# Kernel tuning notes

Hardware: AMD Instinct MI355X
Metric: run time of the kernel (lower is better)

Reference implementation:

```python
import jax, jax.numpy as jnp
import numpy as np


def setup_inputs() -> dict:
    key = jax.random.key(0)
    ks = jax.random.split(key, 9)
    B, S, I, H, O = 64, 2048, 256, 256, 256
    s_g = 1.0 / np.sqrt(I + H)  # torch Linear default init scale
    s_f = 1.0 / np.sqrt(H)
    return {
        "x": jax.random.normal(ks[0], (B, S, I), dtype=jnp.float32),
        "W_r": jax.random.normal(ks[1], (H, I + H), dtype=jnp.float32) * s_g,
        "b_r": jax.random.normal(ks[2], (H,), dtype=jnp.float32) * s_g,
        "W_z": jax.random.normal(ks[3], (H, I + H), dtype=jnp.float32) * s_g,
        "b_z": jax.random.normal(ks[4], (H,), dtype=jnp.float32) * s_g,
        "W_h": jax.random.normal(ks[5], (H, I + H), dtype=jnp.float32) * s_g,
        "b_h": jax.random.normal(ks[6], (H,), dtype=jnp.float32) * s_g,
        "W_fc": jax.random.normal(ks[7], (O, H), dtype=jnp.float32) * s_f,
        "b_fc": jax.random.normal(ks[8], (O,), dtype=jnp.float32) * s_f,
    }


def reference(x, W_r, b_r, W_z, b_z, W_h, b_h, W_fc, b_fc):
    B, S, I = x.shape
    H = W_r.shape[0]
    h0 = jnp.zeros((B, H), dtype=x.dtype)

    def step(h, x_t):
        comb = jnp.concatenate([x_t, h], axis=1)            # [B, I+H]
        r = jax.nn.sigmoid(comb @ W_r.T + b_r)              # reset gate
        z = jax.nn.sigmoid(comb @ W_z.T + b_z)              # update gate
        comb_r = jnp.concatenate([x_t, r * h], axis=1)
        h_tilde = jnp.tanh(comb_r @ W_h.T + b_h)
        h_new = (1.0 - z) * h + z * h_tilde
        return h_new, h_new

    # scan over time (strict sequential dependency), x as [S, B, I]
    h_last, hs = jax.lax.scan(step, h0, jnp.swapaxes(x, 0, 1))
    outputs = jnp.einsum('sbh,oh->bso', hs, W_fc) + b_fc    # [B, S, O]
    return outputs, h_last
```

## Files before the change

### kernel.cpp

```cpp
#include <hip/hip_runtime.h>
#include <hip/hip_bf16.h>
#include <hip/hip_fp16.h>

typedef unsigned short u16;
typedef unsigned int u32;
typedef __attribute__((ext_vector_type(8))) short bf16x8;
typedef __attribute__((ext_vector_type(4))) float f32x4;
typedef _Float16 __attribute__((ext_vector_type(2))) f16x2;

#define MFMA16(a, b, c) __builtin_amdgcn_mfma_f32_16x16x32_bf16((a), (b), (c), 0, 0, 0)

__device__ __forceinline__ float bflo(u32 u) { return __uint_as_float(u << 16); }
__device__ __forceinline__ float bfhi(u32 u) { return __uint_as_float(u & 0xffff0000u); }
__device__ __forceinline__ float bf1(u16 u) { return __uint_as_float(((u32)u) << 16); }
__device__ __forceinline__ u16 f2bf(float f) {
    __hip_bfloat16 b = __float2bfloat16(f);
    return __builtin_bit_cast(u16, b);
}

__device__ __forceinline__ int sniff_fp32(const void* Wr) {
    const uint4* p = (const uint4*)Wr;
    uint4 v = p[threadIdx.x & 15];
    u32 a[4] = {v.x, v.y, v.z, v.w};
    float m = 0.f;
#pragma unroll
    for (int i = 0; i < 4; ++i) {
        float lo = fabsf(bflo(a[i])), hi = fabsf(bfhi(a[i]));
        if (!(lo < 1e30f)) lo = 1e30f;
        if (!(hi < 1e30f)) hi = 1e30f;
        m = fmaxf(m, fmaxf(lo, hi));
    }
#pragma unroll
    for (int off = 32; off; off >>= 1) m = fmaxf(m, __shfl_xor(m, off, 64));
    return m > 100.f ? 1 : 0;
}

__device__ __forceinline__ bf16x8 load8bf(const void* base, size_t idx, int f32) {
    if (f32) {
        const float4* p = (const float4*)((const float*)base + idx);
        float4 v0 = p[0], v1 = p[1];
        bf16x8 r;
        r[0] = (short)f2bf(v0.x); r[1] = (short)f2bf(v0.y);
        r[2] = (short)f2bf(v0.z); r[3] = (short)f2bf(v0.w);
        r[4] = (short)f2bf(v1.x); r[5] = (short)f2bf(v1.y);
        r[6] = (short)f2bf(v1.z); r[7] = (short)f2bf(v1.w);
        return r;
    }
    return *(const bf16x8*)((const u16*)base + idx);
}

__device__ __forceinline__ void load8h(const void* base, size_t idx, int f32, f16x2* dst) {
    if (f32) {
        const float4* p = (const float4*)((const float*)base + idx);
        float4 v0 = p[0], v1 = p[1];
        dst[0] = f16x2{(_Float16)v0.x, (_Float16)v0.y};
        dst[1] = f16x2{(_Float16)v0.z, (_Float16)v0.w};
        dst[2] = f16x2{(_Float16)v1.x, (_Float16)v1.y};
        dst[3] = f16x2{(_Float16)v1.z, (_Float16)v1.w};
    } else {
        uint4 v = *(const uint4*)((const u16*)base + idx);
        dst[0] = f16x2{(_Float16)bflo(v.x), (_Float16)bfhi(v.x)};
        dst[1] = f16x2{(_Float16)bflo(v.y), (_Float16)bfhi(v.y)};
        dst[2] = f16x2{(_Float16)bflo(v.z), (_Float16)bfhi(v.z)};
        dst[3] = f16x2{(_Float16)bflo(v.w), (_Float16)bfhi(v.w)};
    }
}

__device__ __forceinline__ float load1f(const void* base, size_t idx, int f32) {
    return f32 ? ((const float*)base)[idx] : bf1(((const u16*)base)[idx]);
}

__global__ __launch_bounds__(256, 2) void gru_pre(
    const void* __restrict__ x,
    const void* __restrict__ Wr, const void* __restrict__ Wz, const void* __restrict__ Wh,
    const void* __restrict__ br, const void* __restrict__ bz, const void* __restrict__ bh,
    __half* __restrict__ gxc, int s0, int lgSc)
{
    const int f32 = sniff_fp32(Wr);
    const int tid = threadIdx.x;
    const int R0 = blockIdx.x * 64;

    __shared__ __align__(16) u16 As[64][264];

    {
        const int i = tid >> 2;
        const int kq = (tid & 3) * 64;
        const int m = R0 + i;
        const int b = m >> lgSc;
        const int sl = m & ((1 << lgSc) - 1);
        const size_t xbase = ((size_t)(b * 2048 + s0 + sl)) * 256 + kq;
        u16* dst = &As[i][kq];
        if (f32) {
            const float4* p = (const float4*)((const float*)x + xbase);
#pragma unroll
            for (int j = 0; j < 8; ++j) {
                float4 v0 = p[2 * j], v1 = p[2 * j + 1];
                uint4 o;
                o.x = ((u32)f2bf(v0.y) << 16) | f2bf(v0.x);
                o.y = ((u32)f2bf(v0.w) << 16) | f2bf(v0.z);
                o.z = ((u32)f2bf(v1.y) << 16) | f2bf(v1.x);
                o.w = ((u32)f2bf(v1.w) << 16) | f2bf(v1.z);
                *(uint4*)(dst + j * 8) = o;
            }
        } else {
            const uint4* p = (const uint4*)((const u16*)x + xbase);
#pragma unroll
            for (int j = 0; j < 8; ++j) *(uint4*)(dst + j * 8) = p[j];
        }
    }
    __syncthreads();

    const int wv = tid >> 6;
    const int lane = tid & 63;
    const int q = lane >> 4, l16 = lane & 15;

    for (int j = 0; j < 3; ++j) {
        const int gi = wv * 3 + j;
        const int g = gi >> 2;
        const int col0 = (gi & 3) * 64;
        const void* W    = (g == 0) ? Wr : ((g == 1) ? Wz : Wh);
        const void* bias = (g == 0) ? br : ((g == 1) ? bz : bh);
        const size_t wbase = (size_t)(col0 + l16) * 512 + q * 8;

        f32x4 acc[4][4];
#pragma unroll
        for (int mt = 0; mt < 4; ++mt)
#pragma unroll
            for (int nt = 0; nt < 4; ++nt) acc[mt][nt] = (f32x4){0, 0, 0, 0};

#pragma unroll
        for (int k0 = 0; k0 < 256; k0 += 32) {
            bf16x8 bfr[4];
#pragma unroll
            for (int nt = 0; nt < 4; ++nt)
                bfr[nt] = load8bf(W, wbase + (size_t)nt * 16 * 512 + k0, f32);
#pragma unroll
            for (int mt = 0; mt < 4; ++mt) {
                bf16x8 af = *(const bf16x8*)&As[mt * 16 + l16][k0 + q * 8];
#pragma unroll
                for (int nt = 0; nt < 4; ++nt)
                    acc[mt][nt] = MFMA16(af, bfr[nt], acc[mt][nt]);
            }
        }
#pragma unroll
        for (int nt = 0; nt < 4; ++nt) {
            const int col = col0 + nt * 16 + l16;
            const float bv = load1f(bias, col, f32);
#pragma unroll
            for (int mt = 0; mt < 4; ++mt)
#pragma unroll
                for (int r = 0; r < 4; ++r) {
                    const int row = R0 + mt * 16 + q * 4 + r;
                    gxc[(size_t)row * 768 + g * 256 + col] =
                        __float2half(acc[mt][nt][r] + bv);
                }
        }
    }
}

__device__ __forceinline__ float dot256(const f16x2* w, const _Float16* hp) {
    const uint4* hp4 = (const uint4*)hp;
    float a0 = 0.f, a1 = 0.f, a2 = 0.f, a3 = 0.f;
#pragma unroll
    for (int c = 0; c < 32; ++c) {
        uint4 hv = hp4[c];
        f16x2 h0 = __builtin_bit_cast(f16x2, hv.x);
        f16x2 h1 = __builtin_bit_cast(f16x2, hv.y);
        f16x2 h2 = __builtin_bit_cast(f16x2, hv.z);
        f16x2 h3 = __builtin_bit_cast(f16x2, hv.w);
#if __has_builtin(__builtin_amdgcn_fdot2)
        a0 = __builtin_amdgcn_fdot2(w[c * 4 + 0], h0, a0, false);
        a1 = __builtin_amdgcn_fdot2(w[c * 4 + 1], h1, a1, false);
        a2 = __builtin_amdgcn_fdot2(w[c * 4 + 2], h2, a2, false);
        a3 = __builtin_amdgcn_fdot2(w[c * 4 + 3], h3, a3, false);
#else
        a0 += (float)w[c*4+0][0] * (float)h0[0] + (float)w[c*4+0][1] * (float)h0[1];
        a1 += (float)w[c*4+1][0] * (float)h1[0] + (float)w[c*4+1][1] * (float)h1[1];
        a2 += (float)w[c*4+2][0] * (float)h2[0] + (float)w[c*4+2][1] * (float)h2[1];
        a3 += (float)w[c*4+3][0] * (float)h3[0] + (float)w[c*4+3][1] * (float)h3[1];
#endif
    }
    return (a0 + a1) + (a2 + a3);
}

__global__ __launch_bounds__(768, 3) void gru_scan(
    const __half* __restrict__ gxc,
    const void* __restrict__ Wr, const void* __restrict__ Wz, const void* __restrict__ Wh,
    float* __restrict__ h_state,
    void* __restrict__ outbase,
    int s0, int Sc, int first, int last)
{
    const int f32 = sniff_fp32(Wr);
    const int b = blockIdx.x;
    const int tid = threadIdx.x;
    const int g = tid >> 8;
    const int n = tid & 255;

    __shared__ __align__(16) _Float16 h_h[256];
    __shared__ __align__(16) _Float16 rh_h[256];
    __shared__ float h_f[256];
    __shared__ float z_f[256];

    const void* W = (g == 0) ? Wr : ((g == 1) ? Wz : Wh);
    f16x2 w[128];
#pragma unroll
    for (int c = 0; c < 32; ++c)
        load8h(W, (size_t)n * 512 + 256 + c * 8, f32, &w[c * 4]);

    if (g == 0) {
        float h0 = first ? 0.0f : h_state[b * 256 + n];
        h_f[n] = h0;
        h_h[n] = (_Float16)h0;
    }
    __syncthreads();

    const __half* gxp = gxc + (size_t)b * Sc * 768 + g * 256 + n;
    __half cur = gxp[0];

    for (int s = 0; s < Sc; ++s) {
        __half nxt = (s + 1 < Sc) ? gxp[(size_t)(s + 1) * 768] : cur;

        if (g < 2) {
            float acc = dot256(w, h_h);
            float pre = acc + __half2float(cur);
            pre = fminf(fmaxf(pre, -30.0f), 30.0f);
            float val = __fdividef(1.0f, 1.0f + __expf(-pre));
            if (g == 0) rh_h[n] = (_Float16)(val * h_f[n]);
            else        z_f[n] = val;
        }
        __syncthreads();

        if (g == 2) {
            float acc = dot256(w, rh_h);
            float pre = acc + __half2float(cur);
            pre = fminf(fmaxf(pre, -15.0f), 15.0f);
            float e = __expf(2.0f * pre);
            float ht = __fdividef(e - 1.0f, e + 1.0f);
            float hold = h_f[n];
            float zz = z_f[n];
            float hn = hold + zz * (ht - hold);
            h_f[n] = hn;
            h_h[n] = (_Float16)hn;
            const size_t oidx = (size_t)(b * 2048 + s0 + s) * 256 + n;
            if (f32) ((float*)outbase)[oidx] = hn;
            else     ((u16*)outbase)[oidx] = f2bf(hn);
            if (s == Sc - 1) {
                h_state[b * 256 + n] = hn;
                if (last) {
                    const size_t lidx = (size_t)33554432 + b * 256 + n;
                    if (f32) ((float*)outbase)[lidx] = hn;
                    else     ((u16*)outbase)[lidx] = f2bf(hn);
                }
            }
        }
        __syncthreads();
        cur = nxt;
    }
}

__global__ __launch_bounds__(256) void gru_proj(
    const void* __restrict__ Wfc, const void* __restrict__ bfc,
    const void* __restrict__ Wr_for_sniff,
    void* __restrict__ io)
{
    const int f32 = sniff_fp32(Wr_for_sniff);
    const int lane = threadIdx.x & 63;
    const int wave = threadIdx.x >> 6;
    const int q = lane >> 4, l16 = lane & 15;
    const int m0 = blockIdx.x * 64 + wave * 16;
    const size_t aidx = (size_t)(m0 + l16) * 256 + q * 8;
    const size_t widx = (size_t)l16 * 256 + q * 8;
    f32x4 acc[16];
#pragma unroll
    for (int t = 0; t < 16; ++t) acc[t] = (f32x4){0, 0, 0, 0};
#pragma unroll 2
    for (int k0 = 0; k0 < 256; k0 += 32) {
        bf16x8 af = load8bf(io, aidx + k0, f32);
#pragma unroll
        for (int t = 0; t < 16; ++t) {
            bf16x8 bfg = load8bf(Wfc, widx + (size_t)t * 16 * 256 + k0, f32);
            acc[t] = MFMA16(af, bfg, acc[t]);
        }
    }
#pragma unroll
    for (int t = 0; t < 16; ++t) {
        const int col = t * 16 + l16;
        const float bv = load1f(bfc, col, f32);
#pragma unroll
        for (int r = 0; r < 4; ++r) {
            const size_t oidx = (size_t)(m0 + q * 4 + r) * 256 + col;
            float v = acc[t][r] + bv;
            if (f32) ((float*)io)[oidx] = v;
            else     ((u16*)io)[oidx] = f2bf(v);
        }
    }
}

extern "C" void kernel_launch(void* const* d_in, const int* in_sizes, int n_in,
                              void* d_out, int out_size, void* d_ws, size_t ws_size,
                              hipStream_t stream) {
    (void)in_sizes; (void)n_in; (void)out_size;
    const void* x   = d_in[0];
    const void* Wr  = d_in[1];
    const void* br  = d_in[2];
    const void* Wz  = d_in[3];
    const void* bz  = d_in[4];
    const void* Wh  = d_in[5];
    const void* bh  = d_in[6];
    const void* Wfc = d_in[7];
    const void* bfc = d_in[8];

    float* h_state = (float*)d_ws;
    __half* gxc = (__half*)((char*)d_ws + 65536);

    int lgSc = 11;
    while (lgSc > 0 &&
           (size_t)65536 + (((size_t)64 << lgSc) * 768 * 2) > ws_size) --lgSc;
    const int Sc = 1 << lgSc;

    for (int s0 = 0; s0 < 2048; s0 += Sc) {
        gru_pre<<<Sc, 256, 0, stream>>>(x, Wr, Wz, Wh, br, bz, bh, gxc, s0, lgSc);
        gru_scan<<<64, 768, 0, stream>>>(gxc, Wr, Wz, Wh, h_state, d_out,
                                         s0, Sc, (s0 == 0) ? 1 : 0,
                                         (s0 + Sc == 2048) ? 1 : 0);
    }
    gru_proj<<<2048, 256, 0, stream>>>(Wfc, bfc, Wr, d_out);
}
```

Before: 4.120 ms.

## Batch 16 sequences per scan block with fp16 MFMA recurrent matvec

The recurrent scan now handles 16 batch rows per workgroup over 4 blocks, replacing the per-row fdot2 dot products with fp16 MFMA over register-resident weights. The input-gate precompute is laid out time-major so each block can double-buffer the next step's gate inputs into LDS. Hidden states are staged as fp16 in a workspace and projected per chunk. A one-time kernel converts all weights to fp16. Using only 4 workgroups cuts GPU parallelism to a handful of CUs, and switching the precompute from bf16 to fp16 changes numerical behaviour.

New measurement: 14.67 ms. 256% more time.

```diff
diff --git a/kernel.cpp b/kernel.cpp
--- a/kernel.cpp
+++ b/kernel.cpp
@@ -4,11 +4,10 @@
 
 typedef unsigned short u16;
 typedef unsigned int u32;
-typedef __attribute__((ext_vector_type(8))) short bf16x8;
 typedef __attribute__((ext_vector_type(4))) float f32x4;
-typedef _Float16 __attribute__((ext_vector_type(2))) f16x2;
-
-#define MFMA16(a, b, c) __builtin_amdgcn_mfma_f32_16x16x32_bf16((a), (b), (c), 0, 0, 0)
+typedef __attribute__((ext_vector_type(8))) _Float16 f16x8;
+
+#define MFMAH(a, b, c) __builtin_amdgcn_mfma_f32_16x16x32_f16((a), (b), (c), 0, 0, 0)
 
 __device__ __forceinline__ float bflo(u32 u) { return __uint_as_float(u << 16); }
 __device__ __forceinline__ float bfhi(u32 u) { return __uint_as_float(u & 0xffff0000u); }
@@ -17,6 +16,10 @@
     __hip_bfloat16 b = __float2bfloat16(f);
     return __builtin_bit_cast(u16, b);
 }
+__device__ __forceinline__ u16 f2h(float f) { return __builtin_bit_cast(u16, (_Float16)f); }
+__device__ __forceinline__ u32 pk2h(float a, float b) {
+    return (u32)f2h(a) | ((u32)f2h(b) << 16);
+}
 
 __device__ __forceinline__ int sniff_fp32(const void* Wr) {
     const uint4* p = (const uint4*)Wr;
@@ -35,77 +38,80 @@
     return m > 100.f ? 1 : 0;
 }
 
-__device__ __forceinline__ bf16x8 load8bf(const void* base, size_t idx, int f32) {
-    if (f32) {
-        const float4* p = (const float4*)((const float*)base + idx);
-        float4 v0 = p[0], v1 = p[1];
-        bf16x8 r;
-        r[0] = (short)f2bf(v0.x); r[1] = (short)f2bf(v0.y);
-        r[2] = (short)f2bf(v0.z); r[3] = (short)f2bf(v0.w);
-        r[4] = (short)f2bf(v1.x); r[5] = (short)f2bf(v1.y);
-        r[6] = (short)f2bf(v1.z); r[7] = (short)f2bf(v1.w);
-        return r;
-    }
-    return *(const bf16x8*)((const u16*)base + idx);
-}
-
-__device__ __forceinline__ void load8h(const void* base, size_t idx, int f32, f16x2* dst) {
-    if (f32) {
-        const float4* p = (const float4*)((const float*)base + idx);
-        float4 v0 = p[0], v1 = p[1];
-        dst[0] = f16x2{(_Float16)v0.x, (_Float16)v0.y};
-        dst[1] = f16x2{(_Float16)v0.z, (_Float16)v0.w};
-        dst[2] = f16x2{(_Float16)v1.x, (_Float16)v1.y};
-        dst[3] = f16x2{(_Float16)v1.z, (_Float16)v1.w};
-    } else {
-        uint4 v = *(const uint4*)((const u16*)base + idx);
-        dst[0] = f16x2{(_Float16)bflo(v.x), (_Float16)bfhi(v.x)};
-        dst[1] = f16x2{(_Float16)bflo(v.y), (_Float16)bfhi(v.y)};
-        dst[2] = f16x2{(_Float16)bflo(v.z), (_Float16)bfhi(v.z)};
-        dst[3] = f16x2{(_Float16)bflo(v.w), (_Float16)bfhi(v.w)};
-    }
-}
-
 __device__ __forceinline__ float load1f(const void* base, size_t idx, int f32) {
     return f32 ? ((const float*)base)[idx] : bf1(((const u16*)base)[idx]);
 }
 
-__global__ __launch_bounds__(256, 2) void gru_pre(
-    const void* __restrict__ x,
-    const void* __restrict__ Wr, const void* __restrict__ Wz, const void* __restrict__ Wh,
-    const void* __restrict__ br, const void* __restrict__ bz, const void* __restrict__ bh,
-    __half* __restrict__ gxc, int s0, int lgSc)
+__global__ void wconv(const void* __restrict__ Wr, const void* __restrict__ Wz,
+                      const void* __restrict__ Wh, const void* __restrict__ Wfc,
+                      u16* __restrict__ wf16)
 {
     const int f32 = sniff_fp32(Wr);
+    const int gid = blockIdx.x * 256 + threadIdx.x;
+    const int e = gid * 4;
+    const void* src;
+    int off;
+    if (e < 131072)      { src = Wr;  off = e; }
+    else if (e < 262144) { src = Wz;  off = e - 131072; }
+    else if (e < 393216) { src = Wh;  off = e - 262144; }
+    else                 { src = Wfc; off = e - 393216; }
+    uint2 o;
+    if (f32) {
+        float4 v = *(const float4*)((const float*)src + off);
+        o.x = pk2h(v.x, v.y);
+        o.y = pk2h(v.z, v.w);
+    } else {
+        uint2 v = *(const uint2*)((const u16*)src + off);
+        o.x = pk2h(bflo(v.x), bfhi(v.x));
+        o.y = pk2h(bflo(v.y), bfhi(v.y));
+    }
+    *(uint2*)(wf16 + e) = o;
+}
+
+__global__ __launch_bounds__(256, 2) void gru_pre(
+    const void* __restrict__ x, const u16* __restrict__ wf16,
+    const void* __restrict__ br, const void* __restrict__ bz, const void* __restrict__ bh,
+    u16* __restrict__ gxc, int s0, int lgSc, const void* __restrict__ Wsniff)
+{
+    const int f32 = sniff_fp32(Wsniff);
     const int tid = threadIdx.x;
     const int R0 = blockIdx.x * 64;
-
-    __shared__ __align__(16) u16 As[64][264];
+    const int msk = (1 << lgSc) - 1;
+
+    __shared__ __align__(16) _Float16 As[64][264];
 
     {
         const int i = tid >> 2;
         const int kq = (tid & 3) * 64;
         const int m = R0 + i;
         const int b = m >> lgSc;
-        const int sl = m & ((1 << lgSc) - 1);
+        const int sl = m & msk;
         const size_t xbase = ((size_t)(b * 2048 + s0 + sl)) * 256 + kq;
-        u16* dst = &As[i][kq];
+        u16* dst = (u16*)&As[i][kq];
         if (f32) {
             const float4* p = (const float4*)((const float*)x + xbase);
 #pragma unroll
             for (int j = 0; j < 8; ++j) {
                 float4 v0 = p[2 * j], v1 = p[2 * j + 1];
                 uint4 o;
-                o.x = ((u32)f2bf(v0.y) << 16) | f2bf(v0.x);
-                o.y = ((u32)f2bf(v0.w) << 16) | f2bf(v0.z);
-                o.z = ((u32)f2bf(v1.y) << 16) | f2bf(v1.x);
-                o.w = ((u32)f2bf(v1.w) << 16) | f2bf(v1.z);
+                o.x = pk2h(v0.x, v0.y);
+                o.y = pk2h(v0.z, v0.w);
+                o.z = pk2h(v1.x, v1.y);
+                o.w = pk2h(v1.z, v1.w);
                 *(uint4*)(dst + j * 8) = o;
             }
         } else {
             const uint4* p = (const uint4*)((const u16*)x + xbase);
 #pragma unroll
-            for (int j = 0; j < 8; ++j) *(uint4*)(dst + j * 8) = p[j];
+            for (int j = 0; j < 8; ++j) {
+                uint4 v = p[j];
+                uint4 o;
+                o.x = pk2h(bflo(v.x), bfhi(v.x));
+                o.y = pk2h(bflo(v.y), bfhi(v.y));
+                o.z = pk2h(bflo(v.z), bfhi(v.z));
+                o.w = pk2h(bflo(v.w), bfhi(v.w));
+                *(uint4*)(dst + j * 8) = o;
+            }
         }
     }
     __syncthreads();
@@ -118,9 +124,8 @@
         const int gi = wv * 3 + j;
         const int g = gi >> 2;
         const int col0 = (gi & 3) * 64;
-        const void* W    = (g == 0) ? Wr : ((g == 1) ? Wz : Wh);
         const void* bias = (g == 0) ? br : ((g == 1) ? bz : bh);
-        const size_t wbase = (size_t)(col0 + l16) * 512 + q * 8;
+        const size_t wbase = (size_t)(g * 256 + col0 + l16) * 512 + q * 8;
 
         f32x4 acc[4][4];
 #pragma unroll
@@ -130,16 +135,16 @@
 
 #pragma unroll
         for (int k0 = 0; k0 < 256; k0 += 32) {
-            bf16x8 bfr[4];
+            f16x8 bfr[4];
 #pragma unroll
             for (int nt = 0; nt < 4; ++nt)
-                bfr[nt] = load8bf(W, wbase + (size_t)nt * 16 * 512 + k0, f32);
+                bfr[nt] = *(const f16x8*)(wf16 + wbase + (size_t)nt * 8192 + k0);
 #pragma unroll
             for (int mt = 0; mt < 4; ++mt) {
-                bf16x8 af = *(const bf16x8*)&As[mt * 16 + l16][k0 + q * 8];
+                f16x8 af = *(const f16x8*)&As[mt * 16 + l16][k0 + q * 8];
 #pragma unroll
                 for (int nt = 0; nt < 4; ++nt)
-                    acc[mt][nt] = MFMA16(af, bfr[nt], acc[mt][nt]);
+                    acc[mt][nt] = MFMAH(af, bfr[nt], acc[mt][nt]);
             }
         }
 #pragma unroll
@@ -150,123 +155,178 @@
             for (int mt = 0; mt < 4; ++mt)
 #pragma unroll
                 for (int r = 0; r < 4; ++r) {
-                    const int row = R0 + mt * 16 + q * 4 + r;
-                    gxc[(size_t)row * 768 + g * 256 + col] =
-                        __float2half(acc[mt][nt][r] + bv);
+                    const int m = R0 + mt * 16 + q * 4 + r;
+                    const int b = m >> lgSc;
+                    const int sl = m & msk;
+                    gxc[((size_t)sl * 64 + b) * 768 + g * 256 + col] =
+                        f2h(acc[mt][nt][r] + bv);
                 }
         }
     }
 }
 
-__device__ __forceinline__ float dot256(const f16x2* w, const _Float16* hp) {
-    const uint4* hp4 = (const uint4*)hp;
-    float a0 = 0.f, a1 = 0.f, a2 = 0.f, a3 = 0.f;
-#pragma unroll
-    for (int c = 0; c < 32; ++c) {
-        uint4 hv = hp4[c];
-        f16x2 h0 = __builtin_bit_cast(f16x2, hv.x);
-        f16x2 h1 = __builtin_bit_cast(f16x2, hv.y);
-        f16x2 h2 = __builtin_bit_cast(f16x2, hv.z);
-        f16x2 h3 = __builtin_bit_cast(f16x2, hv.w);
-#if __has_builtin(__builtin_amdgcn_fdot2)
-        a0 = __builtin_amdgcn_fdot2(w[c * 4 + 0], h0, a0, false);
-        a1 = __builtin_amdgcn_fdot2(w[c * 4 + 1], h1, a1, false);
-        a2 = __builtin_amdgcn_fdot2(w[c * 4 + 2], h2, a2, false);
-        a3 = __builtin_amdgcn_fdot2(w[c * 4 + 3], h3, a3, false);
-#else
-        a0 += (float)w[c*4+0][0] * (float)h0[0] + (float)w[c*4+0][1] * (float)h0[1];
-        a1 += (float)w[c*4+1][0] * (float)h1[0] + (float)w[c*4+1][1] * (float)h1[1];
-        a2 += (float)w[c*4+2][0] * (float)h2[0] + (float)w[c*4+2][1] * (float)h2[1];
-        a3 += (float)w[c*4+3][0] * (float)h3[0] + (float)w[c*4+3][1] * (float)h3[1];
-#endif
-    }
-    return (a0 + a1) + (a2 + a3);
-}
-
 __global__ __launch_bounds__(768, 3) void gru_scan(
-    const __half* __restrict__ gxc,
-    const void* __restrict__ Wr, const void* __restrict__ Wz, const void* __restrict__ Wh,
+    const u16* __restrict__ gxc,
+    const u16* __restrict__ wf16,
     float* __restrict__ h_state,
+    u16* __restrict__ hs,
     void* __restrict__ outbase,
-    int s0, int Sc, int first, int last)
+    const void* __restrict__ Wsniff,
+    int Sc, int first, int last)
 {
-    const int f32 = sniff_fp32(Wr);
-    const int b = blockIdx.x;
+    const int f32o = sniff_fp32(Wsniff);
     const int tid = threadIdx.x;
-    const int g = tid >> 8;
-    const int n = tid & 255;
-
-    __shared__ __align__(16) _Float16 h_h[256];
-    __shared__ __align__(16) _Float16 rh_h[256];
-    __shared__ float h_f[256];
-    __shared__ float z_f[256];
-
-    const void* W = (g == 0) ? Wr : ((g == 1) ? Wz : Wh);
-    f16x2 w[128];
-#pragma unroll
-    for (int c = 0; c < 32; ++c)
-        load8h(W, (size_t)n * 512 + 256 + c * 8, f32, &w[c * 4]);
-
-    if (g == 0) {
-        float h0 = first ? 0.0f : h_state[b * 256 + n];
-        h_f[n] = h0;
-        h_h[n] = (_Float16)h0;
+    const int wv = tid >> 6, lane = tid & 63;
+    const int q = lane >> 4, l16 = lane & 15;
+    const int gate = wv >> 2;
+    const int wsub = wv & 3;
+    const int b0 = blockIdx.x * 16;
+    const int colb = wsub * 64 + l16;
+
+    __shared__ __align__(16) _Float16 h_h[16][264];
+    __shared__ __align__(16) _Float16 rh_h[16][264];
+    __shared__ __align__(16) float    z_s[16][260];
+    __shared__ __align__(16) float    h_f[16][260];
+    __shared__ __align__(16) _Float16 gxl[2][16][776];
+
+    f16x8 w[4][8];
+#pragma unroll
+    for (int nt = 0; nt < 4; ++nt) {
+        const size_t rowb = (size_t)(gate * 256 + colb + nt * 16) * 512 + 256 + q * 8;
+#pragma unroll
+        for (int kk = 0; kk < 8; ++kk)
+            w[nt][kk] = *(const f16x8*)(wf16 + rowb + kk * 32);
+    }
+
+    if (gate == 2) {
+#pragma unroll
+        for (int nt = 0; nt < 4; ++nt) {
+            const int col = colb + nt * 16;
+#pragma unroll
+            for (int r = 0; r < 4; ++r) {
+                const int b = q * 4 + r;
+                float h0 = first ? 0.f : h_state[(size_t)(b0 + b) * 256 + col];
+                h_f[b][col] = h0;
+                h_h[b][col] = (_Float16)h0;
+            }
+        }
+    }
+    const int tb = tid / 48, tc = (tid % 48) * 16;
+    {
+        const u16* gs = gxc + (size_t)(b0 + tb) * 768 + tc;
+        uint4 a0 = *(const uint4*)gs, a1 = *(const uint4*)(gs + 8);
+        u16* d = (u16*)&gxl[0][tb][tc];
+        *(uint4*)d = a0;
+        *(uint4*)(d + 8) = a1;
     }
     __syncthreads();
 
-    const __half* gxp = gxc + (size_t)b * Sc * 768 + g * 256 + n;
-    __half cur = gxp[0];
+    const size_t gstep = 49152;
+    uint4 pf0 = {0, 0, 0, 0}, pf1 = {0, 0, 0, 0};
 
     for (int s = 0; s < Sc; ++s) {
-        __half nxt = (s + 1 < Sc) ? gxp[(size_t)(s + 1) * 768] : cur;
-
-        if (g < 2) {
-            float acc = dot256(w, h_h);
-            float pre = acc + __half2float(cur);
-            pre = fminf(fmaxf(pre, -30.0f), 30.0f);
-            float val = __fdividef(1.0f, 1.0f + __expf(-pre));
-            if (g == 0) rh_h[n] = (_Float16)(val * h_f[n]);
-            else        z_f[n] = val;
+        const int pc = s & 1;
+        if (s + 1 < Sc) {
+            const u16* gs = gxc + (size_t)(s + 1) * gstep + (size_t)(b0 + tb) * 768 + tc;
+            pf0 = *(const uint4*)gs;
+            pf1 = *(const uint4*)(gs + 8);
+        }
+        if (gate < 2) {
+            if (s > 0) {
+                const int cb = tid >> 5, cc = (tid & 31) * 8;
+                uint4 hv = *(const uint4*)&h_h[cb][cc];
+                *(uint4*)(hs + ((size_t)(b0 + cb) * Sc + (s - 1)) * 256 + cc) = hv;
+            }
+            f32x4 acc[4];
+#pragma unroll
+            for (int nt = 0; nt < 4; ++nt) acc[nt] = (f32x4){0.f, 0.f, 0.f, 0.f};
+#pragma unroll
+            for (int kk = 0; kk < 8; ++kk) {
+                f16x8 a = *(const f16x8*)&h_h[l16][kk * 32 + q * 8];
+#pragma unroll
+                for (int nt = 0; nt < 4; ++nt)
+                    acc[nt] = MFMAH(a, w[nt][kk], acc[nt]);
+            }
+#pragma unroll
+            for (int nt = 0; nt < 4; ++nt) {
+                const int col = colb + nt * 16;
+#pragma unroll
+                for (int r = 0; r < 4; ++r) {
+                    const int b = q * 4 + r;
+                    float p = acc[nt][r] + (float)gxl[pc][b][gate * 256 + col];
+                    float sg = __fdividef(1.f, 1.f + __expf(-p));
+                    if (gate == 0) rh_h[b][col] = (_Float16)(sg * h_f[b][col]);
+                    else           z_s[b][col] = sg;
+                }
+            }
         }
         __syncthreads();
-
-        if (g == 2) {
-            float acc = dot256(w, rh_h);
-            float pre = acc + __half2float(cur);
-            pre = fminf(fmaxf(pre, -15.0f), 15.0f);
-            float e = __expf(2.0f * pre);
-            float ht = __fdividef(e - 1.0f, e + 1.0f);
-            float hold = h_f[n];
-            float zz = z_f[n];
-            float hn = hold + zz * (ht - hold);
-            h_f[n] = hn;
-            h_h[n] = (_Float16)hn;
-            const size_t oidx = (size_t)(b * 2048 + s0 + s) * 256 + n;
-            if (f32) ((float*)outbase)[oidx] = hn;
-            else     ((u16*)outbase)[oidx] = f2bf(hn);
-            if (s == Sc - 1) {
-                h_state[b * 256 + n] = hn;
-                if (last) {
-                    const size_t lidx = (size_t)33554432 + b * 256 + n;
-                    if (f32) ((float*)outbase)[lidx] = hn;
-                    else     ((u16*)outbase)[lidx] = f2bf(hn);
+        if (gate == 2) {
+            f32x4 acc[4];
+#pragma unroll
+            for (int nt = 0; nt < 4; ++nt) acc[nt] = (f32x4){0.f, 0.f, 0.f, 0.f};
+#pragma unroll
+            for (int kk = 0; kk < 8; ++kk) {
+                f16x8 a = *(const f16x8*)&rh_h[l16][kk * 32 + q * 8];
+#pragma unroll
+                for (int nt = 0; nt < 4; ++nt)
+                    acc[nt] = MFMAH(a, w[nt][kk], acc[nt]);
+            }
+#pragma unroll
+            for (int nt = 0; nt < 4; ++nt) {
+                const int col = colb + nt * 16;
+#pragma unroll
+                for (int r = 0; r < 4; ++r) {
+                    const int b = q * 4 + r;
+                    float p = acc[nt][r] + (float)gxl[pc][b][512 + col];
+                    p = fminf(fmaxf(p, -15.f), 15.f);
+                    float e = __expf(2.f * p);
+                    float ht = 1.f - __fdividef(2.f, e + 1.f);
+                    float hold = h_f[b][col];
+                    float hn = fmaf(z_s[b][col], ht - hold, hold);
+                    h_f[b][col] = hn;
+                    h_h[b][col] = (_Float16)hn;
+                    if (s == Sc - 1) {
+                        h_state[(size_t)(b0 + b) * 256 + col] = hn;
+                        if (last) {
+                            const size_t li = (size_t)33554432 + (size_t)(b0 + b) * 256 + col;
+                            if (f32o) ((float*)outbase)[li] = hn;
+                            else      ((u16*)outbase)[li] = f2bf(hn);
+                        }
+                    }
                 }
             }
+            if (s + 1 < Sc) {
+                u16* d = (u16*)&gxl[pc ^ 1][tb][tc];
+                *(uint4*)d = pf0;
+                *(uint4*)(d + 8) = pf1;
+            }
+        } else {
+            if (s + 1 < Sc) {
+                u16* d = (u16*)&gxl[pc ^ 1][tb][tc];
+                *(uint4*)d = pf0;
+                *(uint4*)(d + 8) = pf1;
+            }
         }
         __syncthreads();
-        cur = nxt;
+    }
+    if (tid < 512) {
+        const int cb = tid >> 5, cc = (tid & 31) * 8;
+        uint4 hv = *(const uint4*)&h_h[cb][cc];
+        *(uint4*)(hs + ((size_t)(b0 + cb) * Sc + (Sc - 1)) * 256 + cc) = hv;
     }
 }
 
 __global__ __launch_bounds__(256) void gru_proj(
-    const void* __restrict__ Wfc, const void* __restrict__ bfc,
-    const void* __restrict__ Wr_for_sniff,
-    void* __restrict__ io)
+    const u16* __restrict__ wfc16, const void* __restrict__ bfc,
+    const void* __restrict__ Wsniff, const u16* __restrict__ hs,
+    void* __restrict__ outb, int s0, int lgSc)
 {
-    const int f32 = sniff_fp32(Wr_for_sniff);
+    const int f32 = sniff_fp32(Wsniff);
     const int lane = threadIdx.x & 63;
     const int wave = threadIdx.x >> 6;
     const int q = lane >> 4, l16 = lane & 15;
+    const int msk = (1 << lgSc) - 1;
     const int m0 = blockIdx.x * 64 + wave * 16;
     const size_t aidx = (size_t)(m0 + l16) * 256 + q * 8;
     const size_t widx = (size_t)l16 * 256 + q * 8;
@@ -275,11 +335,11 @@
     for (int t = 0; t < 16; ++t) acc[t] = (f32x4){0, 0, 0, 0};
 #pragma unroll 2
     for (int k0 = 0; k0 < 256; k0 += 32) {
-        bf16x8 af = load8bf(io, aidx + k0, f32);
+        f16x8 af = *(const f16x8*)(hs + aidx + k0);
 #pragma unroll
         for (int t = 0; t < 16; ++t) {
-            bf16x8 bfg = load8bf(Wfc, widx + (size_t)t * 16 * 256 + k0, f32);
-            acc[t] = MFMA16(af, bfg, acc[t]);
+            f16x8 bfg = *(const f16x8*)(wfc16 + widx + (size_t)t * 4096 + k0);
+            acc[t] = MFMAH(af, bfg, acc[t]);
         }
     }
 #pragma unroll
@@ -288,10 +348,13 @@
         const float bv = load1f(bfc, col, f32);
 #pragma unroll
         for (int r = 0; r < 4; ++r) {
-            const size_t oidx = (size_t)(m0 + q * 4 + r) * 256 + col;
+            const int m = m0 + q * 4 + r;
+            const int b = m >> lgSc;
+            const int sl = m & msk;
+            const size_t oidx = ((size_t)b * 2048 + s0 + sl) * 256 + col;
             float v = acc[t][r] + bv;
-            if (f32) ((float*)io)[oidx] = v;
-            else     ((u16*)io)[oidx] = f2bf(v);
+            if (f32) ((float*)outb)[oidx] = v;
+            else     ((u16*)outb)[oidx] = f2bf(v);
         }
     }
 }
@@ -311,18 +374,23 @@
     const void* bfc = d_in[8];
 
     float* h_state = (float*)d_ws;
-    __half* gxc = (__half*)((char*)d_ws + 65536);
+    u16*   wf16    = (u16*)((char*)d_ws + 65536);
 
     int lgSc = 11;
     while (lgSc > 0 &&
-           (size_t)65536 + (((size_t)64 << lgSc) * 768 * 2) > ws_size) --lgSc;
+           (size_t)1048576 + ((size_t)131072 << lgSc) > ws_size) --lgSc;
     const int Sc = 1 << lgSc;
+    u16* gxc = (u16*)((char*)d_ws + 1048576);
+    u16* hs  = (u16*)((char*)d_ws + 1048576 + (size_t)Sc * 98304);
+
+    wconv<<<448, 256, 0, stream>>>(Wr, Wz, Wh, Wfc, wf16);
 
     for (int s0 = 0; s0 < 2048; s0 += Sc) {
-        gru_pre<<<Sc, 256, 0, stream>>>(x, Wr, Wz, Wh, br, bz, bh, gxc, s0, lgSc);
-        gru_scan<<<64, 768, 0, stream>>>(gxc, Wr, Wz, Wh, h_state, d_out,
-                                         s0, Sc, (s0 == 0) ? 1 : 0,
-                                         (s0 + Sc == 2048) ? 1 : 0);
-    }
-    gru_proj<<<2048, 256, 0, stream>>>(Wfc, bfc, Wr, d_out);
-}
+        gru_pre<<<Sc, 256, 0, stream>>>(x, wf16, br, bz, bh, gxc, s0, lgSc, Wr);
+        gru_scan<<<4, 768, 0, stream>>>(gxc, wf16, h_state, hs, d_out, Wr,
+                                        Sc, (s0 == 0) ? 1 : 0,
+                                        (s0 + Sc == 2048) ? 1 : 0);
+        gru_proj<<<Sc, 256, 0, stream>>>(wf16 + 393216, bfc, Wr, hs, d_out,
+                                         s0, lgSc);
+    }
+}
```
